# Kernel tuning notes

Measured on AMD Instinct MI355X. Metric: run time of the kernel, lower is better.

Reference implementation:

```python
import jax, jax.numpy as jnp
import numpy as np

N_NODES, N_EDGES, CH, FEAT = 20000, 320000, 256, 118


def setup_inputs() -> dict:
    key = jax.random.key(0)
    ks = jax.random.split(key, 8)
    x = jax.random.uniform(ks[0], (N_NODES, FEAT), dtype=jnp.float32)
    edge_index = jax.random.randint(ks[1], (2, N_EDGES), 0, N_NODES, dtype=jnp.int64)
    s = 0.05
    W_embed = jax.random.normal(ks[2], (FEAT, CH), dtype=jnp.float32) * s
    b_embed = jnp.zeros((CH,), jnp.float32)
    W1 = jax.random.normal(ks[3], (CH, CH), dtype=jnp.float32) * s
    b1 = jnp.zeros((CH,), jnp.float32)
    W2 = jax.random.normal(ks[4], (CH, CH), dtype=jnp.float32) * s
    b2 = jnp.zeros((CH,), jnp.float32)
    return {"x": x, "edge_index": edge_index, "W_embed": W_embed, "b_embed": b_embed,
            "W1": W1, "b1": b1, "W2": W2, "b2": b2}


def reference(x, edge_index, W_embed, b_embed, W1, b1, W2, b2):
    n = x.shape[0]
    # node embedding: Linear(118 -> C)
    h = x @ W_embed + b_embed  # [N, C]
    src, dst = edge_index[0], edge_index[1]
    # message: gather x_j per edge, dense1 + exact GELU (dropout = identity in eval)
    msg = jax.nn.gelu(h[src] @ W1 + b1, approximate=False)  # [E, C]
    # mean aggregation into destination nodes
    agg = jax.ops.segment_sum(msg, dst, num_segments=n)  # [N, C]
    cnt = jax.ops.segment_sum(jnp.ones((msg.shape[0],), msg.dtype), dst, num_segments=n)
    agg = agg / jnp.maximum(cnt, 1.0)[:, None]
    # update: dense2 + exact GELU
    out = jax.nn.gelu(agg @ W2 + b2, approximate=False)  # [N, C]
    # final mean over channel dim
    return out.mean(axis=1)  # [N]
```

## Files before the change

kernel.cpp:

```cpp
#include <hip/hip_runtime.h>
#include <math.h>

#define N_NODES 20000
#define N_EDGES 320000
#define CH      256
#define FEAT    118
#define KPAD    128
#define CAP     48

typedef float    f32x4 __attribute__((ext_vector_type(4)));
typedef short    s16x8 __attribute__((ext_vector_type(8)));
typedef _Float16 f16x4 __attribute__((ext_vector_type(4)));
typedef unsigned short u16;

union Frag { s16x8 v; u16 u[8]; };

__device__ __forceinline__ float gelu_exact(float x) {
    return 0.5f * x * (1.0f + erff(x * 0.70710678118654752f));
}
__device__ __forceinline__ u16 f2bf(float f) {
    unsigned u = __float_as_uint(f);
    u = (u + 0x7FFFu + ((u >> 16) & 1u)) >> 16;
    return (u16)u;
}
__device__ __forceinline__ float bf2f(u16 h) { return __uint_as_float(((unsigned)h) << 16); }

__global__ __launch_bounds__(256) void pack_x(const float* __restrict__ x,
                                              u16* __restrict__ Ah, u16* __restrict__ Al) {
    int fid = blockIdx.x * 256 + threadIdx.x;
    int lane = fid & 63, ks = (fid >> 6) & 3, mt = fid >> 8;
    int row = mt * 16 + (lane & 15);
    int k0 = ks * 32 + (lane >> 4) * 8;
    Frag hi, lo;
    #pragma unroll
    for (int j = 0; j < 8; j++) {
        int k = k0 + j;
        float v = (k < FEAT) ? x[(size_t)row * FEAT + k] : 0.0f;
        u16 h = f2bf(v);
        hi.u[j] = h; lo.u[j] = f2bf(v - bf2f(h));
    }
    ((s16x8*)Ah)[fid] = hi.v;
    ((s16x8*)Al)[fid] = lo.v;
}

__global__ __launch_bounds__(256) void pack_w(const float* __restrict__ W,
                                              u16* __restrict__ Bh, u16* __restrict__ Bl,
                                              int Krows, int KS) {
    int fid = blockIdx.x * 256 + threadIdx.x;
    int lane = fid & 63;
    int ks = (fid >> 6) & (KS - 1);
    int nt = fid / (64 * KS);
    int n = nt * 16 + (lane & 15);
    int k0 = ks * 32 + (lane >> 4) * 8;
    Frag hi, lo;
    #pragma unroll
    for (int j = 0; j < 8; j++) {
        int k = k0 + j;
        float v = (k < Krows) ? W[(size_t)k * 256 + n] : 0.0f;
        u16 h = f2bf(v);
        hi.u[j] = h; lo.u[j] = f2bf(v - bf2f(h));
    }
    ((s16x8*)Bh)[fid] = hi.v;
    ((s16x8*)Bl)[fid] = lo.v;
}

__global__ __launch_bounds__(256) void fill_bins(const int* __restrict__ ei,
                                                 int* __restrict__ cnt,
                                                 int* __restrict__ bins) {
    int e = blockIdx.x * 256 + threadIdx.x;
    if (e >= N_EDGES) return;
    int s = ei[e];
    int d = ei[N_EDGES + e];
    int p = atomicAdd(&cnt[d], 1);
    if (p < CAP) bins[d * CAP + p] = s;
}

template<int KS>
__device__ __forceinline__ void mm_core(const s16x8* __restrict__ Ah, const s16x8* __restrict__ Al,
                                        const s16x8* __restrict__ Bh, const s16x8* __restrict__ Bl,
                                        int mt0, int nt0, int lane, f32x4 acc[2][4]) {
    #pragma unroll
    for (int ks = 0; ks < KS; ks++) {
        s16x8 a0h = Ah[((size_t)(mt0 + 0) * KS + ks) * 64 + lane];
        s16x8 a0l = Al[((size_t)(mt0 + 0) * KS + ks) * 64 + lane];
        s16x8 a1h = Ah[((size_t)(mt0 + 1) * KS + ks) * 64 + lane];
        s16x8 a1l = Al[((size_t)(mt0 + 1) * KS + ks) * 64 + lane];
        #pragma unroll
        for (int t = 0; t < 4; t++) {
            s16x8 bh = Bh[((size_t)(nt0 + t) * KS + ks) * 64 + lane];
            s16x8 bl = Bl[((size_t)(nt0 + t) * KS + ks) * 64 + lane];
            acc[0][t] = __builtin_amdgcn_mfma_f32_16x16x32_bf16(a0h, bh, acc[0][t], 0, 0, 0);
            acc[0][t] = __builtin_amdgcn_mfma_f32_16x16x32_bf16(a0l, bh, acc[0][t], 0, 0, 0);
            acc[0][t] = __builtin_amdgcn_mfma_f32_16x16x32_bf16(a0h, bl, acc[0][t], 0, 0, 0);
            acc[1][t] = __builtin_amdgcn_mfma_f32_16x16x32_bf16(a1h, bh, acc[1][t], 0, 0, 0);
            acc[1][t] = __builtin_amdgcn_mfma_f32_16x16x32_bf16(a1l, bh, acc[1][t], 0, 0, 0);
            acc[1][t] = __builtin_amdgcn_mfma_f32_16x16x32_bf16(a1h, bl, acc[1][t], 0, 0, 0);
        }
    }
}

__global__ __launch_bounds__(256) void gemm_embed(const u16* __restrict__ Ah_, const u16* __restrict__ Al_,
                                                  const u16* __restrict__ Bh_, const u16* __restrict__ Bl_,
                                                  const float* __restrict__ bias,
                                                  u16* __restrict__ Ch, u16* __restrict__ Cl) {
    __shared__ float Ls[32][266];
    const int tid = threadIdx.x, wave = tid >> 6, lane = tid & 63;
    const int quad = lane >> 4, lm = lane & 15;
    const int mt0 = blockIdx.x * 2, nt0 = wave * 4;
    f32x4 acc[2][4];
    #pragma unroll
    for (int mi = 0; mi < 2; mi++)
        #pragma unroll
        for (int t = 0; t < 4; t++) acc[mi][t] = f32x4{0.f, 0.f, 0.f, 0.f};
    mm_core<4>((const s16x8*)Ah_, (const s16x8*)Al_, (const s16x8*)Bh_, (const s16x8*)Bl_,
               mt0, nt0, lane, acc);
    #pragma unroll
    for (int t = 0; t < 4; t++) {
        float bn = bias[(nt0 + t) * 16 + lm];
        #pragma unroll
        for (int mi = 0; mi < 2; mi++)
            #pragma unroll
            for (int r = 0; r < 4; r++)
                Ls[mi * 16 + quad * 4 + r][(nt0 + t) * 16 + lm] = acc[mi][t][r] + bn;
    }
    __syncthreads();
    #pragma unroll
    for (int it = 0; it < 4; it++) {
        int fid = it * 256 + tid;
        int l = fid & 63, ks = (fid >> 6) & 7, mi = fid >> 9;
        int row = mi * 16 + (l & 15), c0 = ks * 32 + (l >> 4) * 8;
        Frag hi, lo;
        #pragma unroll
        for (int j = 0; j < 8; j++) {
            float v = Ls[row][c0 + j];
            u16 h = f2bf(v);
            hi.u[j] = h; lo.u[j] = f2bf(v - bf2f(h));
        }
        size_t o = ((size_t)(mt0 + mi) * 8 + ks) * 64 + l;
        ((s16x8*)Ch)[o] = hi.v;
        ((s16x8*)Cl)[o] = lo.v;
    }
}

__global__ __launch_bounds__(256) void gemm_hidden(const u16* __restrict__ Ah_, const u16* __restrict__ Al_,
                                                   const u16* __restrict__ Bh_, const u16* __restrict__ Bl_,
                                                   const float* __restrict__ bias,
                                                   _Float16* __restrict__ Mout) {
    __shared__ _Float16 Ls[32][256];
    const int tid = threadIdx.x, wave = tid >> 6, lane = tid & 63;
    const int quad = lane >> 4, lm = lane & 15;
    const int mt0 = blockIdx.x * 2, nt0 = wave * 4;
    f32x4 acc[2][4];
    #pragma unroll
    for (int mi = 0; mi < 2; mi++)
        #pragma unroll
        for (int t = 0; t < 4; t++) acc[mi][t] = f32x4{0.f, 0.f, 0.f, 0.f};
    mm_core<8>((const s16x8*)Ah_, (const s16x8*)Al_, (const s16x8*)Bh_, (const s16x8*)Bl_,
               mt0, nt0, lane, acc);
    #pragma unroll
    for (int t = 0; t < 4; t++) {
        float bn = bias[(nt0 + t) * 16 + lm];
        #pragma unroll
        for (int mi = 0; mi < 2; mi++)
            #pragma unroll
            for (int r = 0; r < 4; r++)
                Ls[mi * 16 + quad * 4 + r][(nt0 + t) * 16 + lm] =
                    (_Float16)gelu_exact(acc[mi][t][r] + bn);
    }
    __syncthreads();
    s16x8* dst = (s16x8*)Mout + (size_t)blockIdx.x * 1024;
    const s16x8* src = (const s16x8*)&Ls[0][0];
    #pragma unroll
    for (int it = 0; it < 4; it++)
        dst[it * 256 + tid] = src[it * 256 + tid];
}

__global__ __launch_bounds__(256) void gemm_mean(const u16* __restrict__ Ah_, const u16* __restrict__ Al_,
                                                 const u16* __restrict__ Bh_, const u16* __restrict__ Bl_,
                                                 const float* __restrict__ bias,
                                                 float* __restrict__ out) {
    __shared__ float part[4][32];
    const int tid = threadIdx.x, wave = tid >> 6, lane = tid & 63;
    const int quad = lane >> 4, lm = lane & 15;
    const int mt0 = blockIdx.x * 2, nt0 = wave * 4;
    f32x4 acc[2][4];
    #pragma unroll
    for (int mi = 0; mi < 2; mi++)
        #pragma unroll
        for (int t = 0; t < 4; t++) acc[mi][t] = f32x4{0.f, 0.f, 0.f, 0.f};
    mm_core<8>((const s16x8*)Ah_, (const s16x8*)Al_, (const s16x8*)Bh_, (const s16x8*)Bl_,
               mt0, nt0, lane, acc);
    float p[2][4] = {{0.f,0.f,0.f,0.f},{0.f,0.f,0.f,0.f}};
    #pragma unroll
    for (int t = 0; t < 4; t++) {
        float bn = bias[(nt0 + t) * 16 + lm];
        #pragma unroll
        for (int mi = 0; mi < 2; mi++)
            #pragma unroll
            for (int r = 0; r < 4; r++)
                p[mi][r] += gelu_exact(acc[mi][t][r] + bn);
    }
    #pragma unroll
    for (int off = 1; off < 16; off <<= 1)
        #pragma unroll
        for (int mi = 0; mi < 2; mi++)
            #pragma unroll
            for (int r = 0; r < 4; r++)
                p[mi][r] += __shfl_xor(p[mi][r], off, 64);
    if (lm == 0)
        #pragma unroll
        for (int mi = 0; mi < 2; mi++)
            #pragma unroll
            for (int r = 0; r < 4; r++)
                part[wave][mi * 16 + quad * 4 + r] = p[mi][r];
    __syncthreads();
    if (tid < 32) {
        float s = part[0][tid] + part[1][tid] + part[2][tid] + part[3][tid];
        out[blockIdx.x * 32 + tid] = s * (1.0f / 256.0f);
    }
}

__global__ __launch_bounds__(256) void aggregate(const _Float16* __restrict__ M,
                                                 const int* __restrict__ cnt,
                                                 const int* __restrict__ bins,
                                                 u16* __restrict__ Ah, u16* __restrict__ Al) {
    int node = (blockIdx.x * 256 + threadIdx.x) >> 6;
    int lane = threadIdx.x & 63;
    int c = cnt[node];
    int cc = min(c, CAP);
    int myid = (lane < CAP) ? bins[node * CAP + lane] : 0;
    float a0 = 0.f, a1 = 0.f, a2 = 0.f, a3 = 0.f;
    for (int j = 0; j < cc; j++) {
        int s = __shfl(myid, j, 64);
        f16x4 v = *(const f16x4*)(M + (size_t)s * CH + lane * 4);
        a0 += (float)v.x; a1 += (float)v.y; a2 += (float)v.z; a3 += (float)v.w;
    }
    float inv = 1.0f / (float)max(c, 1);
    float vv[4] = {a0 * inv, a1 * inv, a2 * inv, a3 * inv};
    int mt = node >> 4, lm = node & 15;
    int ks = lane >> 3, quad = (lane & 7) >> 1, j0 = (lane & 1) * 4;
    size_t base = (((size_t)mt * 8 + ks) * 64 + quad * 16 + lm) * 8 + j0;
    ushort4 hv, lv;
    u16* hp = (u16*)&hv; u16* lp = (u16*)&lv;
    #pragma unroll
    for (int q = 0; q < 4; q++) {
        u16 h = f2bf(vv[q]);
        hp[q] = h; lp[q] = f2bf(vv[q] - bf2f(h));
    }
    *(ushort4*)(Ah + base) = hv;
    *(ushort4*)(Al + base) = lv;
}

extern "C" void kernel_launch(void* const* d_in, const int* in_sizes, int n_in,
                              void* d_out, int out_size, void* d_ws, size_t ws_size,
                              hipStream_t stream) {
    const float* x  = (const float*)d_in[0];
    const int*   ei = (const int*)d_in[1];
    const float* We = (const float*)d_in[2];
    const float* be = (const float*)d_in[3];
    const float* W1 = (const float*)d_in[4];
    const float* b1 = (const float*)d_in[5];
    const float* W2 = (const float*)d_in[6];
    const float* b2 = (const float*)d_in[7];
    float* out = (float*)d_out;

    char* ws = (char*)d_ws;
    u16* xh = (u16*)ws;
    u16* xl = (u16*)(ws + 5120000);
    _Float16* M = (_Float16*)ws;
    size_t off = 10240000;
    u16* hh = (u16*)(ws + off); off += 10240000;
    u16* hl = (u16*)(ws + off); off += 10240000;
    u16* weh = (u16*)(ws + off); off += 65536;
    u16* wel = (u16*)(ws + off); off += 65536;
    u16* w1h = (u16*)(ws + off); off += 131072;
    u16* w1l = (u16*)(ws + off); off += 131072;
    u16* w2h = (u16*)(ws + off); off += 131072;
    u16* w2l = (u16*)(ws + off); off += 131072;
    int* cnt  = (int*)(ws + off); off += N_NODES * 4;
    int* bins = (int*)(ws + off); off += (size_t)N_NODES * CAP * 4;

    hipMemsetAsync(cnt, 0, N_NODES * sizeof(int), stream);
    pack_x<<<1250, 256, 0, stream>>>(x, xh, xl);
    pack_w<<<16, 256, 0, stream>>>(We, weh, wel, FEAT, 4);
    pack_w<<<32, 256, 0, stream>>>(W1, w1h, w1l, CH, 8);
    pack_w<<<32, 256, 0, stream>>>(W2, w2h, w2l, CH, 8);
    fill_bins<<<(N_EDGES + 255) / 256, 256, 0, stream>>>(ei, cnt, bins);

    gemm_embed<<<N_NODES / 32, 256, 0, stream>>>(xh, xl, weh, wel, be, hh, hl);
    gemm_hidden<<<N_NODES / 32, 256, 0, stream>>>(hh, hl, w1h, w1l, b1, M);
    aggregate<<<N_NODES / 4, 256, 0, stream>>>(M, cnt, bins, hh, hl);
    gemm_mean<<<N_NODES / 32, 256, 0, stream>>>(hh, hl, w2h, w2l, b2, out);
}
```

Before: 180.5 us.

## Fold embed into W1, fuse prep kernels, fuse aggregation with final GEMM

Precomputes the combined weight W_embed@W1 and bias b_embed@W1+b1 inside a single prep kernel, so the per-edge-source hidden GEMM runs directly on x with K=128 instead of two chained GEMMs. All packing and edge binning are merged into one launch. Aggregation is fused with the W2 GEMM and mean epilogue through shared memory, which removes the intermediate hh/hl round trip through global memory. The precomputed weight product adds serial dot-product work in the prep blocks and changes rounding slightly.

```diff
diff --git a/kernel.cpp b/kernel.cpp
--- a/kernel.cpp
+++ b/kernel.cpp
@@ -5,7 +5,6 @@
 #define N_EDGES 320000
 #define CH      256
 #define FEAT    118
-#define KPAD    128
 #define CAP     48
 
 typedef float    f32x4 __attribute__((ext_vector_type(4)));
@@ -25,70 +24,103 @@
 }
 __device__ __forceinline__ float bf2f(u16 h) { return __uint_as_float(((unsigned)h) << 16); }
 
-__global__ __launch_bounds__(256) void pack_x(const float* __restrict__ x,
-                                              u16* __restrict__ Ah, u16* __restrict__ Al) {
-    int fid = blockIdx.x * 256 + threadIdx.x;
-    int lane = fid & 63, ks = (fid >> 6) & 3, mt = fid >> 8;
-    int row = mt * 16 + (lane & 15);
-    int k0 = ks * 32 + (lane >> 4) * 8;
-    Frag hi, lo;
-    #pragma unroll
-    for (int j = 0; j < 8; j++) {
-        int k = k0 + j;
-        float v = (k < FEAT) ? x[(size_t)row * FEAT + k] : 0.0f;
-        u16 h = f2bf(v);
-        hi.u[j] = h; lo.u[j] = f2bf(v - bf2f(h));
-    }
-    ((s16x8*)Ah)[fid] = hi.v;
-    ((s16x8*)Al)[fid] = lo.v;
-}
-
-__global__ __launch_bounds__(256) void pack_w(const float* __restrict__ W,
-                                              u16* __restrict__ Bh, u16* __restrict__ Bl,
-                                              int Krows, int KS) {
-    int fid = blockIdx.x * 256 + threadIdx.x;
-    int lane = fid & 63;
-    int ks = (fid >> 6) & (KS - 1);
-    int nt = fid / (64 * KS);
-    int n = nt * 16 + (lane & 15);
-    int k0 = ks * 32 + (lane >> 4) * 8;
-    Frag hi, lo;
-    #pragma unroll
-    for (int j = 0; j < 8; j++) {
-        int k = k0 + j;
-        float v = (k < Krows) ? W[(size_t)k * 256 + n] : 0.0f;
-        u16 h = f2bf(v);
-        hi.u[j] = h; lo.u[j] = f2bf(v - bf2f(h));
-    }
-    ((s16x8*)Bh)[fid] = hi.v;
-    ((s16x8*)Bl)[fid] = lo.v;
-}
-
-__global__ __launch_bounds__(256) void fill_bins(const int* __restrict__ ei,
-                                                 int* __restrict__ cnt,
-                                                 int* __restrict__ bins) {
-    int e = blockIdx.x * 256 + threadIdx.x;
-    if (e >= N_EDGES) return;
-    int s = ei[e];
-    int d = ei[N_EDGES + e];
-    int p = atomicAdd(&cnt[d], 1);
-    if (p < CAP) bins[d * CAP + p] = s;
-}
-
-template<int KS>
-__device__ __forceinline__ void mm_core(const s16x8* __restrict__ Ah, const s16x8* __restrict__ Al,
-                                        const s16x8* __restrict__ Bh, const s16x8* __restrict__ Bl,
-                                        int mt0, int nt0, int lane, f32x4 acc[2][4]) {
-    #pragma unroll
-    for (int ks = 0; ks < KS; ks++) {
-        s16x8 a0h = Ah[((size_t)(mt0 + 0) * KS + ks) * 64 + lane];
-        s16x8 a0l = Al[((size_t)(mt0 + 0) * KS + ks) * 64 + lane];
-        s16x8 a1h = Ah[((size_t)(mt0 + 1) * KS + ks) * 64 + lane];
-        s16x8 a1l = Al[((size_t)(mt0 + 1) * KS + ks) * 64 + lane];
+__global__ __launch_bounds__(256) void prep(const float* __restrict__ x,
+                                            const int* __restrict__ ei,
+                                            const float* __restrict__ We,
+                                            const float* __restrict__ be,
+                                            const float* __restrict__ W1,
+                                            const float* __restrict__ b1,
+                                            const float* __restrict__ W2,
+                                            u16* __restrict__ xh, u16* __restrict__ xl,
+                                            int* __restrict__ cnt, int* __restrict__ bins,
+                                            u16* __restrict__ w2h, u16* __restrict__ w2l,
+                                            u16* __restrict__ wch, u16* __restrict__ wcl,
+                                            float* __restrict__ bc) {
+    const int b = blockIdx.x, tid = threadIdx.x;
+    if (b < 1250) {
+        int fid = b * 256 + tid;
+        int lane = fid & 63, ks = (fid >> 6) & 3, mt = fid >> 8;
+        int row = mt * 16 + (lane & 15);
+        int k0 = ks * 32 + (lane >> 4) * 8;
+        Frag hi, lo;
+        #pragma unroll
+        for (int j = 0; j < 8; j++) {
+            int k = k0 + j;
+            float v = (k < FEAT) ? x[(size_t)row * FEAT + k] : 0.0f;
+            u16 h = f2bf(v);
+            hi.u[j] = h; lo.u[j] = f2bf(v - bf2f(h));
+        }
+        ((s16x8*)xh)[fid] = hi.v;
+        ((s16x8*)xl)[fid] = lo.v;
+    } else if (b < 2500) {
+        int e = (b - 1250) * 256 + tid;
+        int s = ei[e];
+        int d = ei[N_EDGES + e];
+        int p = atomicAdd(&cnt[d], 1);
+        if (p < CAP) bins[(size_t)d * CAP + p] = s;
+    } else if (b < 2532) {
+        int fid = (b - 2500) * 256 + tid;
+        int lane = fid & 63, ks = (fid >> 6) & 7, nt = fid >> 9;
+        int n = nt * 16 + (lane & 15);
+        int k0 = ks * 32 + (lane >> 4) * 8;
+        Frag hi, lo;
+        #pragma unroll
+        for (int j = 0; j < 8; j++) {
+            float v = W2[(size_t)(k0 + j) * 256 + n];
+            u16 h = f2bf(v);
+            hi.u[j] = h; lo.u[j] = f2bf(v - bf2f(h));
+        }
+        ((s16x8*)w2h)[fid] = hi.v;
+        ((s16x8*)w2l)[fid] = lo.v;
+    } else {
+        int f = b - 2532;
+        int n = tid;
+        if (f < 128) {
+            float acc = 0.0f;
+            if (f < FEAT) {
+                const float* wr = We + (size_t)f * 256;
+                #pragma unroll 8
+                for (int c = 0; c < 256; c++) acc += wr[c] * W1[(size_t)c * 256 + n];
+            }
+            int nt = n >> 4, lm = n & 15, ks = f >> 5, q = (f >> 3) & 3, j = f & 7;
+            size_t idx = (((size_t)nt * 4 + ks) * 64 + q * 16 + lm) * 8 + j;
+            u16 h = f2bf(acc);
+            wch[idx] = h;
+            wcl[idx] = f2bf(acc - bf2f(h));
+        } else {
+            float acc = b1[n];
+            #pragma unroll 8
+            for (int c = 0; c < 256; c++) acc += be[c] * W1[(size_t)c * 256 + n];
+            bc[n] = acc;
+        }
+    }
+}
+
+__global__ __launch_bounds__(256) void gemm_main(const u16* __restrict__ Ah_, const u16* __restrict__ Al_,
+                                                 const u16* __restrict__ Bh_, const u16* __restrict__ Bl_,
+                                                 const float* __restrict__ bias,
+                                                 _Float16* __restrict__ Mout) {
+    __shared__ _Float16 Ls[32][256];
+    const int tid = threadIdx.x, wave = tid >> 6, lane = tid & 63;
+    const int quad = lane >> 4, lm = lane & 15;
+    const int mt0 = blockIdx.x * 2, nt0 = wave * 4;
+    const s16x8* Ah = (const s16x8*)Ah_; const s16x8* Al = (const s16x8*)Al_;
+    const s16x8* Bh = (const s16x8*)Bh_; const s16x8* Bl = (const s16x8*)Bl_;
+    f32x4 acc[2][4];
+    #pragma unroll
+    for (int mi = 0; mi < 2; mi++)
+        #pragma unroll
+        for (int t = 0; t < 4; t++) acc[mi][t] = f32x4{0.f, 0.f, 0.f, 0.f};
+    #pragma unroll
+    for (int ks = 0; ks < 4; ks++) {
+        s16x8 a0h = Ah[((size_t)(mt0 + 0) * 4 + ks) * 64 + lane];
+        s16x8 a0l = Al[((size_t)(mt0 + 0) * 4 + ks) * 64 + lane];
+        s16x8 a1h = Ah[((size_t)(mt0 + 1) * 4 + ks) * 64 + lane];
+        s16x8 a1l = Al[((size_t)(mt0 + 1) * 4 + ks) * 64 + lane];
         #pragma unroll
         for (int t = 0; t < 4; t++) {
-            s16x8 bh = Bh[((size_t)(nt0 + t) * KS + ks) * 64 + lane];
-            s16x8 bl = Bl[((size_t)(nt0 + t) * KS + ks) * 64 + lane];
+            s16x8 bh = Bh[((size_t)(nt0 + t) * 4 + ks) * 64 + lane];
+            s16x8 bl = Bl[((size_t)(nt0 + t) * 4 + ks) * 64 + lane];
             acc[0][t] = __builtin_amdgcn_mfma_f32_16x16x32_bf16(a0h, bh, acc[0][t], 0, 0, 0);
             acc[0][t] = __builtin_amdgcn_mfma_f32_16x16x32_bf16(a0l, bh, acc[0][t], 0, 0, 0);
             acc[0][t] = __builtin_amdgcn_mfma_f32_16x16x32_bf16(a0h, bl, acc[0][t], 0, 0, 0);
@@ -97,66 +129,6 @@
             acc[1][t] = __builtin_amdgcn_mfma_f32_16x16x32_bf16(a1h, bl, acc[1][t], 0, 0, 0);
         }
     }
-}
-
-__global__ __launch_bounds__(256) void gemm_embed(const u16* __restrict__ Ah_, const u16* __restrict__ Al_,
-                                                  const u16* __restrict__ Bh_, const u16* __restrict__ Bl_,
-                                                  const float* __restrict__ bias,
-                                                  u16* __restrict__ Ch, u16* __restrict__ Cl) {
-    __shared__ float Ls[32][266];
-    const int tid = threadIdx.x, wave = tid >> 6, lane = tid & 63;
-    const int quad = lane >> 4, lm = lane & 15;
-    const int mt0 = blockIdx.x * 2, nt0 = wave * 4;
-    f32x4 acc[2][4];
-    #pragma unroll
-    for (int mi = 0; mi < 2; mi++)
-        #pragma unroll
-        for (int t = 0; t < 4; t++) acc[mi][t] = f32x4{0.f, 0.f, 0.f, 0.f};
-    mm_core<4>((const s16x8*)Ah_, (const s16x8*)Al_, (const s16x8*)Bh_, (const s16x8*)Bl_,
-               mt0, nt0, lane, acc);
-    #pragma unroll
-    for (int t = 0; t < 4; t++) {
-        float bn = bias[(nt0 + t) * 16 + lm];
-        #pragma unroll
-        for (int mi = 0; mi < 2; mi++)
-            #pragma unroll
-            for (int r = 0; r < 4; r++)
-                Ls[mi * 16 + quad * 4 + r][(nt0 + t) * 16 + lm] = acc[mi][t][r] + bn;
-    }
-    __syncthreads();
-    #pragma unroll
-    for (int it = 0; it < 4; it++) {
-        int fid = it * 256 + tid;
-        int l = fid & 63, ks = (fid >> 6) & 7, mi = fid >> 9;
-        int row = mi * 16 + (l & 15), c0 = ks * 32 + (l >> 4) * 8;
-        Frag hi, lo;
-        #pragma unroll
-        for (int j = 0; j < 8; j++) {
-            float v = Ls[row][c0 + j];
-            u16 h = f2bf(v);
-            hi.u[j] = h; lo.u[j] = f2bf(v - bf2f(h));
-        }
-        size_t o = ((size_t)(mt0 + mi) * 8 + ks) * 64 + l;
-        ((s16x8*)Ch)[o] = hi.v;
-        ((s16x8*)Cl)[o] = lo.v;
-    }
-}
-
-__global__ __launch_bounds__(256) void gemm_hidden(const u16* __restrict__ Ah_, const u16* __restrict__ Al_,
-                                                   const u16* __restrict__ Bh_, const u16* __restrict__ Bl_,
-                                                   const float* __restrict__ bias,
-                                                   _Float16* __restrict__ Mout) {
-    __shared__ _Float16 Ls[32][256];
-    const int tid = threadIdx.x, wave = tid >> 6, lane = tid & 63;
-    const int quad = lane >> 4, lm = lane & 15;
-    const int mt0 = blockIdx.x * 2, nt0 = wave * 4;
-    f32x4 acc[2][4];
-    #pragma unroll
-    for (int mi = 0; mi < 2; mi++)
-        #pragma unroll
-        for (int t = 0; t < 4; t++) acc[mi][t] = f32x4{0.f, 0.f, 0.f, 0.f};
-    mm_core<8>((const s16x8*)Ah_, (const s16x8*)Al_, (const s16x8*)Bh_, (const s16x8*)Bl_,
-               mt0, nt0, lane, acc);
     #pragma unroll
     for (int t = 0; t < 4; t++) {
         float bn = bias[(nt0 + t) * 16 + lm];
@@ -175,21 +147,91 @@
         dst[it * 256 + tid] = src[it * 256 + tid];
 }
 
-__global__ __launch_bounds__(256) void gemm_mean(const u16* __restrict__ Ah_, const u16* __restrict__ Al_,
-                                                 const u16* __restrict__ Bh_, const u16* __restrict__ Bl_,
-                                                 const float* __restrict__ bias,
-                                                 float* __restrict__ out) {
+#define LP 272
+__global__ __launch_bounds__(256) void agg_mean(const _Float16* __restrict__ M,
+                                                const int* __restrict__ cnt,
+                                                const int* __restrict__ bins,
+                                                const u16* __restrict__ Bh_, const u16* __restrict__ Bl_,
+                                                const float* __restrict__ bias,
+                                                float* __restrict__ out) {
+    __shared__ u16 Lh[32][LP];
+    __shared__ u16 Ll[32][LP];
     __shared__ float part[4][32];
     const int tid = threadIdx.x, wave = tid >> 6, lane = tid & 63;
     const int quad = lane >> 4, lm = lane & 15;
-    const int mt0 = blockIdx.x * 2, nt0 = wave * 4;
-    f32x4 acc[2][4];
+
+    {
+        int nb = blockIdx.x * 32 + wave * 8;
+        int cfull[8], cc[8], myid[8];
+        #pragma unroll
+        for (int i = 0; i < 8; i++) {
+            cfull[i] = cnt[nb + i];
+            cc[i] = min(cfull[i], CAP);
+            myid[i] = (lane < CAP) ? bins[(size_t)(nb + i) * CAP + lane] : 0;
+        }
+        float acc[8][4];
+        #pragma unroll
+        for (int i = 0; i < 8; i++)
+            #pragma unroll
+            for (int q = 0; q < 4; q++) acc[i][q] = 0.0f;
+        int mx = 0;
+        #pragma unroll
+        for (int i = 0; i < 8; i++) mx = max(mx, cc[i]);
+        for (int j = 0; j < mx; j++) {
+            #pragma unroll
+            for (int i = 0; i < 8; i++) {
+                if (j < cc[i]) {
+                    int s = __shfl(myid[i], j, 64);
+                    f16x4 v = *(const f16x4*)(M + (size_t)s * CH + lane * 4);
+                    acc[i][0] += (float)v.x; acc[i][1] += (float)v.y;
+                    acc[i][2] += (float)v.z; acc[i][3] += (float)v.w;
+                }
+            }
+        }
+        #pragma unroll
+        for (int i = 0; i < 8; i++) {
+            float inv = 1.0f / (float)max(cfull[i], 1);
+            int row = wave * 8 + i;
+            ushort4 hv, lv;
+            u16* hp = (u16*)&hv; u16* lp = (u16*)&lv;
+            #pragma unroll
+            for (int q = 0; q < 4; q++) {
+                float v = acc[i][q] * inv;
+                u16 h = f2bf(v);
+                hp[q] = h; lp[q] = f2bf(v - bf2f(h));
+            }
+            *(ushort4*)&Lh[row][lane * 4] = hv;
+            *(ushort4*)&Ll[row][lane * 4] = lv;
+        }
+    }
+    __syncthreads();
+
+    const int nt0 = wave * 4;
+    const s16x8* Bh = (const s16x8*)Bh_; const s16x8* Bl = (const s16x8*)Bl_;
+    f32x4 acc2[2][4];
     #pragma unroll
     for (int mi = 0; mi < 2; mi++)
         #pragma unroll
-        for (int t = 0; t < 4; t++) acc[mi][t] = f32x4{0.f, 0.f, 0.f, 0.f};
-    mm_core<8>((const s16x8*)Ah_, (const s16x8*)Al_, (const s16x8*)Bh_, (const s16x8*)Bl_,
-               mt0, nt0, lane, acc);
+        for (int t = 0; t < 4; t++) acc2[mi][t] = f32x4{0.f, 0.f, 0.f, 0.f};
+    #pragma unroll
+    for (int ks = 0; ks < 8; ks++) {
+        int c0 = ks * 32 + quad * 8;
+        s16x8 a0h = *(const s16x8*)&Lh[lm][c0];
+        s16x8 a0l = *(const s16x8*)&Ll[lm][c0];
+        s16x8 a1h = *(const s16x8*)&Lh[16 + lm][c0];
+        s16x8 a1l = *(const s16x8*)&Ll[16 + lm][c0];
+        #pragma unroll
+        for (int t = 0; t < 4; t++) {
+            s16x8 bh = Bh[((size_t)(nt0 + t) * 8 + ks) * 64 + lane];
+            s16x8 bl = Bl[((size_t)(nt0 + t) * 8 + ks) * 64 + lane];
+            acc2[0][t] = __builtin_amdgcn_mfma_f32_16x16x32_bf16(a0h, bh, acc2[0][t], 0, 0, 0);
+            acc2[0][t] = __builtin_amdgcn_mfma_f32_16x16x32_bf16(a0l, bh, acc2[0][t], 0, 0, 0);
+            acc2[0][t] = __builtin_amdgcn_mfma_f32_16x16x32_bf16(a0h, bl, acc2[0][t], 0, 0, 0);
+            acc2[1][t] = __builtin_amdgcn_mfma_f32_16x16x32_bf16(a1h, bh, acc2[1][t], 0, 0, 0);
+            acc2[1][t] = __builtin_amdgcn_mfma_f32_16x16x32_bf16(a1l, bh, acc2[1][t], 0, 0, 0);
+            acc2[1][t] = __builtin_amdgcn_mfma_f32_16x16x32_bf16(a1h, bl, acc2[1][t], 0, 0, 0);
+        }
+    }
     float p[2][4] = {{0.f,0.f,0.f,0.f},{0.f,0.f,0.f,0.f}};
     #pragma unroll
     for (int t = 0; t < 4; t++) {
@@ -198,7 +240,7 @@
         for (int mi = 0; mi < 2; mi++)
             #pragma unroll
             for (int r = 0; r < 4; r++)
-                p[mi][r] += gelu_exact(acc[mi][t][r] + bn);
+                p[mi][r] += gelu_exact(acc2[mi][t][r] + bn);
     }
     #pragma unroll
     for (int off = 1; off < 16; off <<= 1)
@@ -218,37 +260,6 @@
         float s = part[0][tid] + part[1][tid] + part[2][tid] + part[3][tid];
         out[blockIdx.x * 32 + tid] = s * (1.0f / 256.0f);
     }
-}
-
-__global__ __launch_bounds__(256) void aggregate(const _Float16* __restrict__ M,
-                                                 const int* __restrict__ cnt,
-                                                 const int* __restrict__ bins,
-                                                 u16* __restrict__ Ah, u16* __restrict__ Al) {
-    int node = (blockIdx.x * 256 + threadIdx.x) >> 6;
-    int lane = threadIdx.x & 63;
-    int c = cnt[node];
-    int cc = min(c, CAP);
-    int myid = (lane < CAP) ? bins[node * CAP + lane] : 0;
-    float a0 = 0.f, a1 = 0.f, a2 = 0.f, a3 = 0.f;
-    for (int j = 0; j < cc; j++) {
-        int s = __shfl(myid, j, 64);
-        f16x4 v = *(const f16x4*)(M + (size_t)s * CH + lane * 4);
-        a0 += (float)v.x; a1 += (float)v.y; a2 += (float)v.z; a3 += (float)v.w;
-    }
-    float inv = 1.0f / (float)max(c, 1);
-    float vv[4] = {a0 * inv, a1 * inv, a2 * inv, a3 * inv};
-    int mt = node >> 4, lm = node & 15;
-    int ks = lane >> 3, quad = (lane & 7) >> 1, j0 = (lane & 1) * 4;
-    size_t base = (((size_t)mt * 8 + ks) * 64 + quad * 16 + lm) * 8 + j0;
-    ushort4 hv, lv;
-    u16* hp = (u16*)&hv; u16* lp = (u16*)&lv;
-    #pragma unroll
-    for (int q = 0; q < 4; q++) {
-        u16 h = f2bf(vv[q]);
-        hp[q] = h; lp[q] = f2bf(vv[q] - bf2f(h));
-    }
-    *(ushort4*)(Ah + base) = hv;
-    *(ushort4*)(Al + base) = lv;
 }
 
 extern "C" void kernel_launch(void* const* d_in, const int* in_sizes, int n_in,
@@ -265,30 +276,21 @@
     float* out = (float*)d_out;
 
     char* ws = (char*)d_ws;
-    u16* xh = (u16*)ws;
-    u16* xl = (u16*)(ws + 5120000);
-    _Float16* M = (_Float16*)ws;
-    size_t off = 10240000;
-    u16* hh = (u16*)(ws + off); off += 10240000;
-    u16* hl = (u16*)(ws + off); off += 10240000;
-    u16* weh = (u16*)(ws + off); off += 65536;
-    u16* wel = (u16*)(ws + off); off += 65536;
-    u16* w1h = (u16*)(ws + off); off += 131072;
-    u16* w1l = (u16*)(ws + off); off += 131072;
+    size_t off = 0;
+    u16* xh = (u16*)(ws + off); off += 5120000;
+    u16* xl = (u16*)(ws + off); off += 5120000;
+    _Float16* M = (_Float16*)(ws + off); off += 10240000;
+    u16* wch = (u16*)(ws + off); off += 65536;
+    u16* wcl = (u16*)(ws + off); off += 65536;
     u16* w2h = (u16*)(ws + off); off += 131072;
     u16* w2l = (u16*)(ws + off); off += 131072;
+    float* bc = (float*)(ws + off); off += 1024;
     int* cnt  = (int*)(ws + off); off += N_NODES * 4;
     int* bins = (int*)(ws + off); off += (size_t)N_NODES * CAP * 4;
 
     hipMemsetAsync(cnt, 0, N_NODES * sizeof(int), stream);
-    pack_x<<<1250, 256, 0, stream>>>(x, xh, xl);
-    pack_w<<<16, 256, 0, stream>>>(We, weh, wel, FEAT, 4);
-    pack_w<<<32, 256, 0, stream>>>(W1, w1h, w1l, CH, 8);
-    pack_w<<<32, 256, 0, stream>>>(W2, w2h, w2l, CH, 8);
-    fill_bins<<<(N_EDGES + 255) / 256, 256, 0, stream>>>(ei, cnt, bins);
-
-    gemm_embed<<<N_NODES / 32, 256, 0, stream>>>(xh, xl, weh, wel, be, hh, hl);
-    gemm_hidden<<<N_NODES / 32, 256, 0, stream>>>(hh, hl, w1h, w1l, b1, M);
-    aggregate<<<N_NODES / 4, 256, 0, stream>>>(M, cnt, bins, hh, hl);
-    gemm_mean<<<N_NODES / 32, 256, 0, stream>>>(hh, hl, w2h, w2l, b2, out);
-}
+    prep<<<2661, 256, 0, stream>>>(x, ei, We, be, W1, b1, W2,
+                                   xh, xl, cnt, bins, w2h, w2l, wch, wcl, bc);
+    gemm_main<<<N_NODES / 32, 256, 0, stream>>>(xh, xl, wch, wcl, bc, M);
+    agg_mean<<<N_NODES / 32, 256, 0, stream>>>(M, cnt, bins, w2h, w2l, b2, out);
+}
```

After: 178.3 us. Within noise of the previous version (-1.3%).
